# Kernel tuning notes

Hardware: AMD Instinct MI355X
Metric: run time of the kernel (lower is better)

The kernel has to match this reference:

```python
import jax, jax.numpy as jnp
import numpy as np

B, H, LQ, LKV, D = 2, 4, 512, 512, 64


def setup_inputs() -> dict:
    key = jax.random.key(0)
    ks = jax.random.split(key, 6)
    queries = jax.random.normal(ks[0], (B, H, LQ, D), dtype=jnp.float32)
    keys = jax.random.normal(ks[1], (B, H, LKV, D), dtype=jnp.float32)
    values = jax.random.normal(ks[2], (B, H, LKV, D), dtype=jnp.float32)
    mask = jax.random.randint(ks[3], (B, LQ, LKV), 0, 2) > 0  # bool [B, Lq, Lkv]
    # linear_concat: weight [D, 2D] (normal std=0.02), bias zeros
    W_concat = jax.random.normal(ks[4], (D, 2 * D), dtype=jnp.float32) * 0.02
    b_concat = jnp.zeros((D,), dtype=jnp.float32)
    # linear_logit: weight [1, D] -> vector [D], bias scalar zero
    w_logit = jax.random.normal(ks[5], (D,), dtype=jnp.float32) * 0.02
    b_logit = jnp.zeros((), dtype=jnp.float32)
    return dict(queries=queries, keys=keys, values=values, mask=mask,
                W_concat=W_concat, b_concat=b_concat,
                w_logit=w_logit, b_logit=b_logit)


def reference(queries, keys, values, mask, W_concat, b_concat, w_logit, b_logit):
    d = queries.shape[-1]
    # cat(q, k) @ W.T == q @ W[:, :d].T + k @ W[:, d:].T  (exact split of the concat-linear)
    qp = jnp.einsum('bhqd,ed->bhqe', queries, W_concat[:, :d])   # [B,H,Lq,D]
    kp = jnp.einsum('bhkd,ed->bhke', keys, W_concat[:, d:])      # [B,H,Lkv,D]
    combined = jnp.tanh(qp[:, :, :, None, :] + kp[:, :, None, :, :] + b_concat)  # [B,H,Lq,Lkv,D]
    logits = jnp.einsum('bhqke,e->bhqk', combined, w_logit) + b_logit            # [B,H,Lq,Lkv]
    # mask handling: invert; rows fully masked get un-masked (avoid all -inf softmax)
    inv = ~mask  # [B,Lq,Lkv]
    inv = jnp.where(jnp.all(inv, axis=-1, keepdims=True), False, inv)
    inv = inv[:, None, :, :]  # broadcast over heads
    logits = jnp.where(inv, -jnp.inf, logits)
    weights = jax.nn.softmax(logits, axis=-1)
    if weights.shape[1] == 1:  # torch .squeeze(dim=1) semantics
        weights = jnp.squeeze(weights, axis=1)
    return weights
```

## Files before the change

### kernel.cpp

```cpp
#include <hip/hip_runtime.h>
#include <hip/hip_bf16.h>


#define NQROWS 4096

__global__ __launch_bounds__(256) void proj_kernel(
    const float* __restrict__ Q, const float* __restrict__ K,
    const float* __restrict__ W, const float* __restrict__ bC,
    float* __restrict__ eq, float* __restrict__ ekt)
{
  const int t  = threadIdx.x;
  const int tr = t >> 6;
  const int e  = t & 63;
  const int rbase = blockIdx.x * 16;
  const bool isK = rbase >= NQROWS;
  const int r0 = isK ? rbase - NQROWS : rbase;
  const float* __restrict__ src = isK ? K : Q;
  const int off = isK ? 64 : 0;

  __shared__ float  srow[16][64];
  __shared__ float4 wsh[64][16];

  for (int i = t; i < 16 * 64; i += 256)
    srow[i >> 6][i & 63] = src[(r0 + (i >> 6)) * 64 + (i & 63)];
  for (int i = t; i < 64 * 16; i += 256) {
    const int er = i >> 4, d4 = i & 15;
    wsh[er][d4 ^ (er & 7)] =
        reinterpret_cast<const float4*>(W + er * 128 + off)[d4];
  }
  __syncthreads();

  float acc0 = 0.f, acc1 = 0.f, acc2 = 0.f, acc3 = 0.f;
  const int rA = tr * 4;
  #pragma unroll
  for (int d4 = 0; d4 < 16; ++d4) {
    const float4 w4 = wsh[e][d4 ^ (e & 7)];
    const float4 s0 = *reinterpret_cast<const float4*>(&srow[rA + 0][d4 * 4]);
    const float4 s1 = *reinterpret_cast<const float4*>(&srow[rA + 1][d4 * 4]);
    const float4 s2 = *reinterpret_cast<const float4*>(&srow[rA + 2][d4 * 4]);
    const float4 s3 = *reinterpret_cast<const float4*>(&srow[rA + 3][d4 * 4]);
    acc0 = fmaf(s0.x, w4.x, acc0); acc0 = fmaf(s0.y, w4.y, acc0);
    acc0 = fmaf(s0.z, w4.z, acc0); acc0 = fmaf(s0.w, w4.w, acc0);
    acc1 = fmaf(s1.x, w4.x, acc1); acc1 = fmaf(s1.y, w4.y, acc1);
    acc1 = fmaf(s1.z, w4.z, acc1); acc1 = fmaf(s1.w, w4.w, acc1);
    acc2 = fmaf(s2.x, w4.x, acc2); acc2 = fmaf(s2.y, w4.y, acc2);
    acc2 = fmaf(s2.z, w4.z, acc2); acc2 = fmaf(s2.w, w4.w, acc2);
    acc3 = fmaf(s3.x, w4.x, acc3); acc3 = fmaf(s3.y, w4.y, acc3);
    acc3 = fmaf(s3.z, w4.z, acc3); acc3 = fmaf(s3.w, w4.w, acc3);
  }

  const float C2 = 2.8853900817779268f;
  if (!isK) {
    const float bias = bC[e];
    eq[(r0 + rA + 0) * 64 + e] = __builtin_amdgcn_exp2f((acc0 + bias) * C2);
    eq[(r0 + rA + 1) * 64 + e] = __builtin_amdgcn_exp2f((acc1 + bias) * C2);
    eq[(r0 + rA + 2) * 64 + e] = __builtin_amdgcn_exp2f((acc2 + bias) * C2);
    eq[(r0 + rA + 3) * 64 + e] = __builtin_amdgcn_exp2f((acc3 + bias) * C2);
  } else {
    const int bh = (r0 + rA) >> 9;
    const int k0 = (r0 + rA) & 511;
    float* __restrict__ dst = ekt + bh * 64 * 512 + e * 512 + k0;
    dst[0] = __builtin_amdgcn_exp2f(acc0 * C2);
    dst[1] = __builtin_amdgcn_exp2f(acc1 * C2);
    dst[2] = __builtin_amdgcn_exp2f(acc2 * C2);
    dst[3] = __builtin_amdgcn_exp2f(acc3 * C2);
  }
}

__global__ __launch_bounds__(512) void attn_kernel(
    const float* __restrict__ eq, const float* __restrict__ ekt,
    const float* __restrict__ wl, const int* __restrict__ mask,
    float* __restrict__ out)
{
  const int t  = threadIdx.x;
  const int w  = t >> 6;
  const int tk = t & 63;
  const int rw = w >> 1;
  const int h  = w & 1;
  const int bh = blockIdx.x >> 7;
  const int qb = blockIdx.x & 127;
  const int b  = bh >> 2;
  const int q  = qb * 4 + rw;

  __shared__ float qsh[4][64];
  __shared__ float w2s[64];
  __shared__ float s_any[8], s_mmax[8], s_rmax[8], s_sum[8];

  if (t < 64) w2s[t] = -2.0f * wl[t];
  if (h == 0) qsh[rw][tk] = eq[(bh * 512 + q) * 64 + tk];
  __syncthreads();

  const float4* __restrict__ kq =
      reinterpret_cast<const float4*>(ekt + bh * 64 * 512) + h * 64 + tk;

  float4 acc = {0.f, 0.f, 0.f, 0.f};

#define QUADC(C)                                                              \
  {                                                                           \
    const float t0 = fmaf(q4.x, K0.C, 1.f);                                   \
    const float t1 = fmaf(q4.y, K1.C, 1.f);                                   \
    const float t2 = fmaf(q4.z, K2.C, 1.f);                                   \
    const float t3 = fmaf(q4.w, K3.C, 1.f);                                   \
    const float t01 = t0 * t1, t23 = t2 * t3;                                 \
    const float den = t01 * t23;                                              \
    const float n01 = fmaf(w4.x, t1, w4.y * t0);                              \
    const float n23 = fmaf(w4.z, t3, w4.w * t2);                              \
    const float num = fmaf(n01, t23, n23 * t01);                              \
    acc.C = fmaf(num, __builtin_amdgcn_rcpf(den), acc.C);                     \
  }

  #pragma unroll 2
  for (int eb = 0; eb < 16; ++eb) {
    const float4 q4 = *reinterpret_cast<const float4*>(&qsh[rw][eb * 4]);
    const float4 w4 = *reinterpret_cast<const float4*>(&w2s[eb * 4]);
    const float4 K0 = kq[(eb * 4 + 0) * 128];
    const float4 K1 = kq[(eb * 4 + 1) * 128];
    const float4 K2 = kq[(eb * 4 + 2) * 128];
    const float4 K3 = kq[(eb * 4 + 3) * 128];
    QUADC(x) QUADC(y) QUADC(z) QUADC(w)
  }

  const int* __restrict__ mrow = mask + (b * 512 + q) * 512 + h * 256;
  const int4 mv = *reinterpret_cast<const int4*>(mrow + 4 * tk);
  const int lo = mv.x | mv.y | mv.z | mv.w;
  const float hany = __any(lo != 0) ? 1.0f : 0.0f;

  const float NEG = -__builtin_inff();
  float4 am = acc;
  if (mv.x == 0) am.x = NEG;
  if (mv.y == 0) am.y = NEG;
  if (mv.z == 0) am.z = NEG;
  if (mv.w == 0) am.w = NEG;

  float rmax = fmaxf(fmaxf(acc.x, acc.y), fmaxf(acc.z, acc.w));
  float mmax = fmaxf(fmaxf(am.x, am.y), fmaxf(am.z, am.w));
  #pragma unroll
  for (int s = 1; s < 64; s <<= 1) {
    rmax = fmaxf(rmax, __shfl_xor(rmax, s));
    mmax = fmaxf(mmax, __shfl_xor(mmax, s));
  }
  if (tk == 0) { s_any[w] = hany; s_mmax[w] = mmax; s_rmax[w] = rmax; }
  __syncthreads();

  const int wp = w & ~1;
  const bool rowany = (s_any[wp] + s_any[wp + 1]) > 0.0f;
  const float m = rowany ? fmaxf(s_mmax[wp], s_mmax[wp + 1])
                         : fmaxf(s_rmax[wp], s_rmax[wp + 1]);
  const float4 av = rowany ? am : acc;

  const float L2E = 1.4426950408889634f;
  const float c = m * L2E;
  float4 p;
  p.x = __builtin_amdgcn_exp2f(fmaf(av.x, L2E, -c));
  p.y = __builtin_amdgcn_exp2f(fmaf(av.y, L2E, -c));
  p.z = __builtin_amdgcn_exp2f(fmaf(av.z, L2E, -c));
  p.w = __builtin_amdgcn_exp2f(fmaf(av.w, L2E, -c));
  float sum = p.x + p.y + p.z + p.w;
  #pragma unroll
  for (int s = 1; s < 64; s <<= 1) sum += __shfl_xor(sum, s);
  if (tk == 0) s_sum[w] = sum;
  __syncthreads();

  const float inv = 1.0f / (s_sum[wp] + s_sum[wp + 1]);
  float4 o4 = {p.x * inv, p.y * inv, p.z * inv, p.w * inv};
  float* __restrict__ o = out + (bh * 512 + q) * 512 + h * 256;
  *reinterpret_cast<float4*>(o + 4 * tk) = o4;
}

extern "C" void kernel_launch(void* const* d_in, const int* in_sizes, int n_in,
                              void* d_out, int out_size, void* d_ws, size_t ws_size,
                              hipStream_t stream) {
  const float* Q  = (const float*)d_in[0];
  const float* K  = (const float*)d_in[1];
  const int*   M  = (const int*)d_in[3];
  const float* W  = (const float*)d_in[4];
  const float* bC = (const float*)d_in[5];
  const float* wl = (const float*)d_in[6];
  float* out = (float*)d_out;
  float* eqbuf  = (float*)d_ws;
  float* ektbuf = eqbuf + NQROWS * 64;

  proj_kernel<<<512, 256, 0, stream>>>(Q, K, W, bC, eqbuf, ektbuf);
  attn_kernel<<<1024, 512, 0, stream>>>(eqbuf, ektbuf, wl, M, out);
}
```

Baseline: 30.65 us.

## Halve proj tile, transpose K output via LDS, prefetch K in attention loop

The projection kernel now processes 8 rows per block across twice as many blocks, and stages the exponentiated K projections in shared memory so the transposed store writes contiguous runs instead of strided scalars. The attention kernel interleaves block indices so neighbouring blocks share a batch-head K tile, issues the mask load before the first barrier, and software-pipelines the K loads one step ahead with the loop fully unrolled. It also adds an occupancy hint to launch bounds. These changes target memory latency and uncoalesced stores, at the cost of more registers and an extra barrier in the projection kernel.

```diff
diff --git a/kernel.cpp b/kernel.cpp
--- a/kernel.cpp
+++ b/kernel.cpp
@@ -12,16 +12,17 @@
   const int t  = threadIdx.x;
   const int tr = t >> 6;
   const int e  = t & 63;
-  const int rbase = blockIdx.x * 16;
+  const int rbase = blockIdx.x * 8;
   const bool isK = rbase >= NQROWS;
   const int r0 = isK ? rbase - NQROWS : rbase;
   const float* __restrict__ src = isK ? K : Q;
   const int off = isK ? 64 : 0;
 
-  __shared__ float  srow[16][64];
+  __shared__ float  srow[8][64];
   __shared__ float4 wsh[64][16];
+  __shared__ float  trsp[64][9];
 
-  for (int i = t; i < 16 * 64; i += 256)
+  for (int i = t; i < 8 * 64; i += 256)
     srow[i >> 6][i & 63] = src[(r0 + (i >> 6)) * 64 + (i & 63)];
   for (int i = t; i < 64 * 16; i += 256) {
     const int er = i >> 4, d4 = i & 15;
@@ -30,23 +31,17 @@
   }
   __syncthreads();
 
-  float acc0 = 0.f, acc1 = 0.f, acc2 = 0.f, acc3 = 0.f;
-  const int rA = tr * 4;
+  float acc0 = 0.f, acc1 = 0.f;
+  const int rA = tr * 2;
   #pragma unroll
   for (int d4 = 0; d4 < 16; ++d4) {
     const float4 w4 = wsh[e][d4 ^ (e & 7)];
     const float4 s0 = *reinterpret_cast<const float4*>(&srow[rA + 0][d4 * 4]);
     const float4 s1 = *reinterpret_cast<const float4*>(&srow[rA + 1][d4 * 4]);
-    const float4 s2 = *reinterpret_cast<const float4*>(&srow[rA + 2][d4 * 4]);
-    const float4 s3 = *reinterpret_cast<const float4*>(&srow[rA + 3][d4 * 4]);
     acc0 = fmaf(s0.x, w4.x, acc0); acc0 = fmaf(s0.y, w4.y, acc0);
     acc0 = fmaf(s0.z, w4.z, acc0); acc0 = fmaf(s0.w, w4.w, acc0);
     acc1 = fmaf(s1.x, w4.x, acc1); acc1 = fmaf(s1.y, w4.y, acc1);
     acc1 = fmaf(s1.z, w4.z, acc1); acc1 = fmaf(s1.w, w4.w, acc1);
-    acc2 = fmaf(s2.x, w4.x, acc2); acc2 = fmaf(s2.y, w4.y, acc2);
-    acc2 = fmaf(s2.z, w4.z, acc2); acc2 = fmaf(s2.w, w4.w, acc2);
-    acc3 = fmaf(s3.x, w4.x, acc3); acc3 = fmaf(s3.y, w4.y, acc3);
-    acc3 = fmaf(s3.z, w4.z, acc3); acc3 = fmaf(s3.w, w4.w, acc3);
   }
 
   const float C2 = 2.8853900817779268f;
@@ -54,20 +49,23 @@
     const float bias = bC[e];
     eq[(r0 + rA + 0) * 64 + e] = __builtin_amdgcn_exp2f((acc0 + bias) * C2);
     eq[(r0 + rA + 1) * 64 + e] = __builtin_amdgcn_exp2f((acc1 + bias) * C2);
-    eq[(r0 + rA + 2) * 64 + e] = __builtin_amdgcn_exp2f((acc2 + bias) * C2);
-    eq[(r0 + rA + 3) * 64 + e] = __builtin_amdgcn_exp2f((acc3 + bias) * C2);
   } else {
-    const int bh = (r0 + rA) >> 9;
-    const int k0 = (r0 + rA) & 511;
-    float* __restrict__ dst = ekt + bh * 64 * 512 + e * 512 + k0;
-    dst[0] = __builtin_amdgcn_exp2f(acc0 * C2);
-    dst[1] = __builtin_amdgcn_exp2f(acc1 * C2);
-    dst[2] = __builtin_amdgcn_exp2f(acc2 * C2);
-    dst[3] = __builtin_amdgcn_exp2f(acc3 * C2);
+    trsp[e][rA + 0] = __builtin_amdgcn_exp2f(acc0 * C2);
+    trsp[e][rA + 1] = __builtin_amdgcn_exp2f(acc1 * C2);
+    __syncthreads();
+    const int bh = r0 >> 9;
+    const int k0 = r0 & 511;
+    float* __restrict__ dst = ekt + bh * 64 * 512 + k0;
+    #pragma unroll
+    for (int iter = 0; iter < 2; ++iter) {
+      const int i  = t + iter * 256;
+      const int e2 = i >> 3, kk = i & 7;
+      dst[e2 * 512 + kk] = trsp[e2][kk];
+    }
   }
 }
 
-__global__ __launch_bounds__(512) void attn_kernel(
+__global__ __launch_bounds__(512, 8) void attn_kernel(
     const float* __restrict__ eq, const float* __restrict__ ekt,
     const float* __restrict__ wl, const int* __restrict__ mask,
     float* __restrict__ out)
@@ -77,8 +75,8 @@
   const int tk = t & 63;
   const int rw = w >> 1;
   const int h  = w & 1;
-  const int bh = blockIdx.x >> 7;
-  const int qb = blockIdx.x & 127;
+  const int bh = blockIdx.x & 7;
+  const int qb = blockIdx.x >> 3;
   const int b  = bh >> 2;
   const int q  = qb * 4 + rw;
 
@@ -88,6 +86,10 @@
 
   if (t < 64) w2s[t] = -2.0f * wl[t];
   if (h == 0) qsh[rw][tk] = eq[(bh * 512 + q) * 64 + tk];
+
+  const int* __restrict__ mrow = mask + (b * 512 + q) * 512 + h * 256;
+  const int4 mv = *reinterpret_cast<const int4*>(mrow + 4 * tk);
+
   __syncthreads();
 
   const float4* __restrict__ kq =
@@ -109,19 +111,24 @@
     acc.C = fmaf(num, __builtin_amdgcn_rcpf(den), acc.C);                     \
   }
 
-  #pragma unroll 2
-  for (int eb = 0; eb < 16; ++eb) {
+  float4 K0 = kq[0 * 128], K1 = kq[1 * 128], K2 = kq[2 * 128], K3 = kq[3 * 128];
+  #pragma unroll
+  for (int eb = 0; eb < 15; ++eb) {
+    const float4 N0 = kq[(eb * 4 + 4) * 128];
+    const float4 N1 = kq[(eb * 4 + 5) * 128];
+    const float4 N2 = kq[(eb * 4 + 6) * 128];
+    const float4 N3 = kq[(eb * 4 + 7) * 128];
     const float4 q4 = *reinterpret_cast<const float4*>(&qsh[rw][eb * 4]);
     const float4 w4 = *reinterpret_cast<const float4*>(&w2s[eb * 4]);
-    const float4 K0 = kq[(eb * 4 + 0) * 128];
-    const float4 K1 = kq[(eb * 4 + 1) * 128];
-    const float4 K2 = kq[(eb * 4 + 2) * 128];
-    const float4 K3 = kq[(eb * 4 + 3) * 128];
+    QUADC(x) QUADC(y) QUADC(z) QUADC(w)
+    K0 = N0; K1 = N1; K2 = N2; K3 = N3;
+  }
+  {
+    const float4 q4 = *reinterpret_cast<const float4*>(&qsh[rw][60]);
+    const float4 w4 = *reinterpret_cast<const float4*>(&w2s[60]);
     QUADC(x) QUADC(y) QUADC(z) QUADC(w)
   }
 
-  const int* __restrict__ mrow = mask + (b * 512 + q) * 512 + h * 256;
-  const int4 mv = *reinterpret_cast<const int4*>(mrow + 4 * tk);
   const int lo = mv.x | mv.y | mv.z | mv.w;
   const float hany = __any(lo != 0) ? 1.0f : 0.0f;
 
@@ -180,6 +187,6 @@
   float* eqbuf  = (float*)d_ws;
   float* ektbuf = eqbuf + NQROWS * 64;
 
-  proj_kernel<<<512, 256, 0, stream>>>(Q, K, W, bC, eqbuf, ektbuf);
+  proj_kernel<<<1024, 256, 0, stream>>>(Q, K, W, bC, eqbuf, ektbuf);
   attn_kernel<<<1024, 512, 0, stream>>>(eqbuf, ektbuf, wl, M, out);
 }
```

Result: faster. 29.72 us (-3.0%).
